# Performance work log

Measured on AMD Instinct MI355X. Metric: run time of the kernel, lower is better.

Reference implementation:

```python
import jax, jax.numpy as jnp
import numpy as np

NUM_HEADS = 16
NEG_INF = -1e18


def setup_inputs() -> dict:
    key = jax.random.key(0)
    ks = jax.random.split(key, 9)
    T, B, D = 2048, 2, 1024
    s = 1.0 / np.sqrt(D)
    return {
        "query": jax.random.normal(ks[0], (T, B, D), jnp.float32),
        "q_w": jax.random.normal(ks[1], (D, D), jnp.float32) * s,
        "q_b": jax.random.normal(ks[2], (D,), jnp.float32) * 0.02,
        "k_w": jax.random.normal(ks[3], (D, D), jnp.float32) * s,
        "k_b": jax.random.normal(ks[4], (D,), jnp.float32) * 0.02,
        "v_w": jax.random.normal(ks[5], (D, D), jnp.float32) * s,
        "v_b": jax.random.normal(ks[6], (D,), jnp.float32) * 0.02,
        "out_w": jax.random.normal(ks[7], (D, D), jnp.float32) * s,
        "out_b": jax.random.normal(ks[8], (D,), jnp.float32) * 0.02,
    }


def reference(query, q_w, q_b, k_w, k_b, v_w, v_b, out_w, out_b):
    # query: [T, B, D] (Time x Batch x Channel). Self-attention, causal mask,
    # dropout=0, need_weights=True.
    T, B, D = query.shape
    H = NUM_HEADS
    hd = D // H
    scaling = 1.0 / jnp.sqrt(jnp.asarray(hd, query.dtype))

    q = (query @ q_w.T + q_b) * scaling
    k = query @ k_w.T + k_b
    v = query @ v_w.T + v_b

    def split_heads(x):  # [T, B, D] -> [B, H, T, hd]
        return x.reshape(T, B, H, hd).transpose(1, 2, 0, 3)

    qh, kh, vh = split_heads(q), split_heads(k), split_heads(v)

    # scores: [B, H, T, T]
    scores = jnp.einsum("bhtd,bhsd->bhts", qh, kh)
    causal = jnp.triu(jnp.full((T, T), NEG_INF, dtype=scores.dtype), k=1)
    scores = scores + causal

    probs = jax.nn.softmax(scores, axis=-1)
    attn = jnp.einsum("bhts,bhsd->bhtd", probs, vh)  # [B, H, T, hd]
    attn = attn.transpose(2, 0, 1, 3).reshape(T, B, D)
    out = attn @ out_w.T + out_b

    # averaged attention weights over heads: [B, T, T]
    avg_weights = probs.sum(axis=1) / H
    return out, avg_weights
```

## Files before the change

### kernel.cpp

```cpp
#include <hip/hip_runtime.h>
#include <hip/hip_bf16.h>
#include <stdint.h>

typedef __hip_bfloat16 bf16;
using short8 = __attribute__((ext_vector_type(8))) short;
using f32x4  = __attribute__((ext_vector_type(4))) float;

#define TDIM 2048
#define BDIM 2
#define DDIM 1024
#define HNUM 16
#define HD   64
#define MDIM 4096
#define M0   16.0f

__device__ __forceinline__ f32x4 mfma16(short8 a, short8 b, f32x4 c) {
  return __builtin_amdgcn_mfma_f32_16x16x32_bf16(a, b, c, 0, 0, 0);
}

union S8 { short8 v; bf16 h[8]; };

__device__ __forceinline__ void gload16(const bf16* g, bf16* l) {
  __builtin_amdgcn_global_load_lds(
      (const __attribute__((address_space(1))) unsigned int*)g,
      (__attribute__((address_space(3))) unsigned int*)l, 16, 0, 0);
}

__global__ __launch_bounds__(256) void cast_all_kernel(
    const float* __restrict__ q, const float* __restrict__ wq,
    const float* __restrict__ wk, const float* __restrict__ wv,
    const float* __restrict__ wo, bf16* __restrict__ dst) {
  int t4 = blockIdx.x * blockDim.x + threadIdx.x;
  int idx = t4 * 4;
  const float* s;
  if (idx < 4194304)      s = q  + idx;
  else if (idx < 5242880) s = wq + (idx - 4194304);
  else if (idx < 6291456) s = wk + (idx - 5242880);
  else if (idx < 7340032) s = wv + (idx - 6291456);
  else                    s = wo + (idx - 7340032);
  float4 v = *(const float4*)s;
  union { ushort4 u; bf16 b[4]; } pk;
  pk.b[0] = __float2bfloat16(v.x);
  pk.b[1] = __float2bfloat16(v.y);
  pk.b[2] = __float2bfloat16(v.z);
  pk.b[3] = __float2bfloat16(v.w);
  *(ushort4*)(dst + idx) = pk.u;
}

__global__ __launch_bounds__(256) void qkv_kernel(
    const bf16* __restrict__ X, const bf16* __restrict__ Wq,
    const bf16* __restrict__ Wk, const bf16* __restrict__ Wv,
    const float* __restrict__ qb, const float* __restrict__ kb,
    const float* __restrict__ vb, bf16* __restrict__ Qo,
    bf16* __restrict__ Ko, bf16* __restrict__ Vto) {
  __shared__ bf16 Xs[128][64];
  __shared__ bf16 Qs[64][64];
  __shared__ bf16 Ks[64][64];
  __shared__ bf16 Vs[64][64];
  const int tid = threadIdx.x, lane = tid & 63, wave = tid >> 6;
  const int m0 = blockIdx.y * 128, n0 = blockIdx.x * 64;
  const int wm = (wave >> 1) * 64, wn = (wave & 1) * 32;
  const int fr = lane & 15, quad = lane >> 4, q8 = quad * 8;
  const int lr = lane >> 3, lc = (lane & 7) * 8;
  f32x4 aq[4][2] = {}, ak[4][2] = {}, av[2][4] = {};
  for (int k0 = 0; k0 < DDIM; k0 += 64) {
    if (k0) __syncthreads();
#pragma unroll
    for (int p = 0; p < 10; p++) {
      int pid = wave * 10 + p;
      const bf16* g;
      bf16* l;
      if (pid < 16) {
        g = X + (size_t)(m0 + pid * 8 + lr) * DDIM + k0 + lc;
        l = &Xs[pid * 8][0];
      } else if (pid < 24) {
        int r = (pid - 16) * 8;
        g = Wq + (size_t)(n0 + r + lr) * DDIM + k0 + lc;
        l = &Qs[r][0];
      } else if (pid < 32) {
        int r = (pid - 24) * 8;
        g = Wk + (size_t)(n0 + r + lr) * DDIM + k0 + lc;
        l = &Ks[r][0];
      } else {
        int r = (pid - 32) * 8;
        g = Wv + (size_t)(n0 + r + lr) * DDIM + k0 + lc;
        l = &Vs[r][0];
      }
      gload16(g, l);
    }
    __syncthreads();
#pragma unroll
    for (int kk = 0; kk < 2; kk++) {
      const int ko = kk * 32 + q8;
      short8 xf[4], qf[2], kf[2], vf[2];
#pragma unroll
      for (int i = 0; i < 4; i++)
        xf[i] = *(const short8*)&Xs[wm + i * 16 + fr][ko];
#pragma unroll
      for (int j = 0; j < 2; j++) {
        qf[j] = *(const short8*)&Qs[wn + j * 16 + fr][ko];
        kf[j] = *(const short8*)&Ks[wn + j * 16 + fr][ko];
        vf[j] = *(const short8*)&Vs[wn + j * 16 + fr][ko];
      }
#pragma unroll
      for (int i = 0; i < 4; i++)
#pragma unroll
        for (int j = 0; j < 2; j++) {
          aq[i][j] = mfma16(xf[i], qf[j], aq[i][j]);
          ak[i][j] = mfma16(xf[i], kf[j], ak[i][j]);
          av[j][i] = mfma16(vf[j], xf[i], av[j][i]);
        }
    }
  }
#pragma unroll
  for (int i = 0; i < 4; i++)
#pragma unroll
    for (int j = 0; j < 2; j++)
#pragma unroll
      for (int r = 0; r < 4; r++) {
        {
          int gm = m0 + wm + i * 16 + quad * 4 + r;
          int gn = n0 + wn + j * 16 + fr;
          int t = gm >> 1, bb = gm & 1, h = gn >> 6, e = gn & 63;
          size_t o = ((size_t)(bb * HNUM + h) * TDIM + t) * HD + e;
          Qo[o] = __float2bfloat16((aq[i][j][r] + qb[gn]) * 0.125f);
          Ko[o] = __float2bfloat16(ak[i][j][r] + kb[gn]);
        }
        {
          int gf = n0 + wn + j * 16 + quad * 4 + r;
          int gt = m0 + wm + i * 16 + fr;
          int t = gt >> 1, bb = gt & 1, h = gf >> 6, e = gf & 63;
          Vto[((size_t)(bb * HNUM + h) * HD + e) * TDIM + t] =
              __float2bfloat16(av[j][i][r] + vb[gf]);
        }
      }
}

__global__ __launch_bounds__(256) void gemm_out_kernel(
    const bf16* __restrict__ P0, const bf16* __restrict__ P1,
    const bf16* __restrict__ Bw, const float* __restrict__ l0buf,
    const float* __restrict__ l1buf, const float* __restrict__ bias,
    float* __restrict__ of32) {
  __shared__ bf16 As[64][40];
  __shared__ bf16 Bs[64][40];
  __shared__ float sInv[64][16];
  const int tid  = threadIdx.x;
  const int lane = tid & 63, wave = tid >> 6;
  const int m0 = blockIdx.y * 64, n0 = blockIdx.x * 64;
  const int wm = (wave >> 1) * 32, wn = (wave & 1) * 32;
  const int fr = lane & 15, quad = lane >> 4, q8 = quad * 8;
  const int ldr = tid >> 2, ldc = (tid & 3) * 8;
#pragma unroll
  for (int e = 0; e < 4; e++) {
    int idx = tid * 4 + e;
    int row = idx >> 4, h = idx & 15;
    int gm = m0 + row, t = gm >> 1, bb = gm & 1;
    size_t li = (size_t)(bb * HNUM + h) * TDIM + t;
    sInv[row][h] = 1.0f / (l0buf[li] + l1buf[li]);
  }
  __syncthreads();
  f32x4 acc[2][2] = {};
  const size_t arow = (size_t)(m0 + ldr) * DDIM + ldc;
  const bf16* bptr = Bw + (size_t)(n0 + ldr) * DDIM + ldc;
  for (int k0 = 0; k0 < DDIM; k0 += 32) {
    S8 a0, a1, apk;
    a0.v = *(const short8*)&P0[arow + k0];
    a1.v = *(const short8*)&P1[arow + k0];
    uint4 bvv = *(const uint4*)(bptr + k0);
    float inv = sInv[ldr][k0 >> 6];
#pragma unroll
    for (int k = 0; k < 8; k++)
      apk.h[k] = __float2bfloat16(
          (__bfloat162float(a0.h[k]) + __bfloat162float(a1.h[k])) * inv);
    __syncthreads();
    *(short8*)&As[ldr][ldc] = apk.v;
    *(uint4*)&Bs[ldr][ldc] = bvv;
    __syncthreads();
    short8 af[2], bfr[2];
    af[0]  = *(const short8*)&As[wm + fr][q8];
    af[1]  = *(const short8*)&As[wm + 16 + fr][q8];
    bfr[0] = *(const short8*)&Bs[wn + fr][q8];
    bfr[1] = *(const short8*)&Bs[wn + 16 + fr][q8];
    acc[0][0] = mfma16(af[0], bfr[0], acc[0][0]);
    acc[0][1] = mfma16(af[0], bfr[1], acc[0][1]);
    acc[1][0] = mfma16(af[1], bfr[0], acc[1][0]);
    acc[1][1] = mfma16(af[1], bfr[1], acc[1][1]);
  }
#pragma unroll
  for (int mt = 0; mt < 2; mt++)
#pragma unroll
    for (int nt = 0; nt < 2; nt++)
#pragma unroll
      for (int i = 0; i < 4; i++) {
        int gm = m0 + wm + mt * 16 + quad * 4 + i;
        int gn = n0 + wn + nt * 16 + fr;
        of32[(size_t)gm * DDIM + gn] = acc[mt][nt][i] + bias[gn];
      }
}

__global__ __launch_bounds__(256) void attn_split_kernel(
    const bf16* __restrict__ Q, const bf16* __restrict__ K,
    const bf16* __restrict__ Vt, bf16* __restrict__ P0o,
    bf16* __restrict__ P1o, float* __restrict__ l0buf,
    float* __restrict__ l1buf) {
  __shared__ bf16 Ks[2][64][40];
  __shared__ bf16 Vs[2][64][40];
  __shared__ bf16 pt[4][16][72];
  const int tid = threadIdx.x, lane = tid & 63, wave = tid >> 6;
  const int bid = blockIdx.x;
  const int part = bid & 1, bh = (bid >> 1) & 31, t64 = 31 - (bid >> 6);
  const int b = bh >> 4, h = bh & 15;
  const int t0 = t64 * 64 + wave * 16;
  const int fr = lane & 15, quad = lane >> 4, q8 = quad * 8;
  const bf16* Qp = Q + ((size_t)bh * TDIM + t0) * HD;
  const bf16* Kp = K + (size_t)bh * TDIM * HD;
  const bf16* Vp = Vt + (size_t)bh * HD * TDIM;
  short8 aq0 = *(const short8*)&Qp[fr * HD + q8];
  short8 aq1 = *(const short8*)&Qp[fr * HD + 32 + q8];
  const int Cb = t64 + 1, C0 = Cb >> 1;
  const int clo = part ? C0 : 0, chi = part ? Cb : C0;
  const int sr0 = tid >> 3, scc = (tid & 7) * 8, sr1 = sr0 + 32;
  const int ssub = scc >> 5, scol = scc & 31;
  f32x4 oacc[4] = {};
  float lsum[4] = {0.f, 0.f, 0.f, 0.f};
  uint4 kv0, kv1, vv0, vv1;
  auto ldglob = [&](int c) {
    int s0 = c * 64;
    kv0 = *(const uint4*)&Kp[(size_t)(s0 + sr0) * HD + scc];
    kv1 = *(const uint4*)&Kp[(size_t)(s0 + sr1) * HD + scc];
    vv0 = *(const uint4*)&Vp[(size_t)sr0 * TDIM + s0 + scc];
    vv1 = *(const uint4*)&Vp[(size_t)sr1 * TDIM + s0 + scc];
  };
  if (clo < chi) ldglob(clo);
  for (int c = clo; c < chi; c++) {
    __syncthreads();
    *(uint4*)&Ks[ssub][sr0][scol] = kv0;
    *(uint4*)&Ks[ssub][sr1][scol] = kv1;
    *(uint4*)&Vs[ssub][sr0][scol] = vv0;
    *(uint4*)&Vs[ssub][sr1][scol] = vv1;
    __syncthreads();
    if (c + 1 < chi) ldglob(c + 1);
    const int s0 = c * 64;
    f32x4 sc[4] = {};
#pragma unroll
    for (int j = 0; j < 4; j++) {
      short8 b0 = *(const short8*)&Ks[0][j * 16 + fr][q8];
      short8 b1 = *(const short8*)&Ks[1][j * 16 + fr][q8];
      sc[j] = mfma16(aq0, b0, sc[j]);
      sc[j] = mfma16(aq1, b1, sc[j]);
    }
#pragma unroll
    for (int j = 0; j < 4; j++) {
      int s_col = s0 + j * 16 + fr;
#pragma unroll
      for (int i = 0; i < 4; i++) {
        float p = 0.f;
        if (s_col <= t0 + quad * 4 + i) {
          p = __expf(sc[j][i] - M0);
          lsum[i] += p;
        }
        pt[wave][quad * 4 + i][j * 16 + fr] = __float2bfloat16(p);
      }
    }
    short8 ap0 = *(const short8*)&pt[wave][fr][q8];
    short8 ap1 = *(const short8*)&pt[wave][fr][32 + q8];
#pragma unroll
    for (int nt = 0; nt < 4; nt++) {
      short8 v0 = *(const short8*)&Vs[0][nt * 16 + fr][q8];
      short8 v1 = *(const short8*)&Vs[1][nt * 16 + fr][q8];
      oacc[nt] = mfma16(ap0, v0, oacc[nt]);
      oacc[nt] = mfma16(ap1, v1, oacc[nt]);
    }
  }
  float lr[4];
#pragma unroll
  for (int i = 0; i < 4; i++) {
    float l = lsum[i];
#pragma unroll
    for (int off = 1; off < 16; off <<= 1) l += __shfl_xor(l, off, 16);
    lr[i] = l;
  }
  bf16*  Op = part ? P1o : P0o;
  float* lb = part ? l1buf : l0buf;
#pragma unroll
  for (int nt = 0; nt < 4; nt++)
#pragma unroll
    for (int i = 0; i < 4; i++) {
      int t_row = t0 + quad * 4 + i;
      int col = h * HD + nt * 16 + fr;
      Op[((size_t)t_row * BDIM + b) * DDIM + col] = __float2bfloat16(oacc[nt][i]);
    }
  if (fr == 0) {
    float4 v = make_float4(lr[0], lr[1], lr[2], lr[3]);
    *(float4*)&lb[(size_t)bh * TDIM + t0 + quad * 4] = v;
  }
}

__global__ __launch_bounds__(256) void avg_kernel(
    const bf16* __restrict__ Q, const bf16* __restrict__ K,
    const float* __restrict__ l0buf, const float* __restrict__ l1buf,
    float* __restrict__ avgw) {
  const int tid = threadIdx.x;
  int r = blockIdx.x;
  const int b = (r >= 2048) ? 1 : 0;
  r &= 2047;
  float* avp = avgw + (size_t)b * TDIM * TDIM;
  if (r >= 1056) {
    int r2 = r - 1056;
    int ti = 0;
    while (ti < 31 && (ti + 1) * (62 - ti) <= r2) ti++;
    int si = (2 * ti + 2) + (r2 - ti * (63 - ti));
    int t0b = ti * 64, s0 = si * 32;
#pragma unroll
    for (int k = 0; k < 2; k++) {
      int off = (tid * 2 + k) * 4;
      *(float4*)&avp[(size_t)(t0b + (off >> 5)) * TDIM + s0 + (off & 31)] =
          make_float4(0.f, 0.f, 0.f, 0.f);
    }
    return;
  }
  int ti = 0;
  while ((ti + 1) * (ti + 2) <= r) ti++;
  const int si = r - ti * (ti + 1);
  const int t0b = ti * 64, s0 = si * 32;

  __shared__ bf16 Qs[2][64][40];
  __shared__ bf16 Ks2[2][32][40];
  __shared__ float sinvl[HNUM][64];
#pragma unroll
  for (int k = 0; k < 4; k++) {
    int idx = tid + k * 256;
    size_t li = (size_t)(b * HNUM + (idx >> 6)) * TDIM + t0b + (idx & 63);
    sinvl[idx >> 6][idx & 63] = 1.0f / (l0buf[li] + l1buf[li]);
  }
  const int lane = tid & 63, wave = tid >> 6;
  const int fr = lane & 15, quad = lane >> 4, q8 = quad * 8;
  const int twr = wave * 16;
  const int qr0 = tid >> 3, qcc = (tid & 7) * 8, qr1 = qr0 + 32;
  const int qsub = qcc >> 5, qcol = qcc & 31;
  const bf16* Qb = Q + (size_t)b * HNUM * TDIM * HD;
  const bf16* Kb = K + (size_t)b * HNUM * TDIM * HD;
  uint4 qv0, qv1, kv1;
  auto ldh = [&](int hh) {
    const bf16* Qh = Qb + (size_t)hh * TDIM * HD;
    const bf16* Kh = Kb + (size_t)hh * TDIM * HD;
    qv0 = *(const uint4*)&Qh[(size_t)(t0b + qr0) * HD + qcc];
    qv1 = *(const uint4*)&Qh[(size_t)(t0b + qr1) * HD + qcc];
    kv1 = *(const uint4*)&Kh[(size_t)(s0 + (qr0 & 31)) * HD + qcc];
  };
  ldh(0);
  f32x4 facc[2] = {};
  for (int hh = 0; hh < HNUM; hh++) {
    __syncthreads();
    *(uint4*)&Qs[qsub][qr0][qcol] = qv0;
    *(uint4*)&Qs[qsub][qr1][qcol] = qv1;
    if (qr0 < 32) *(uint4*)&Ks2[qsub][qr0][qcol] = kv1;
    else          *(uint4*)&Ks2[qsub][qr0 - 32][qcol] = kv1;
    __syncthreads();
    if (hh + 1 < HNUM) ldh(hh + 1);
    short8 a0 = *(const short8*)&Qs[0][twr + fr][q8];
    short8 a1 = *(const short8*)&Qs[1][twr + fr][q8];
#pragma unroll
    for (int nt = 0; nt < 2; nt++) {
      short8 b0 = *(const short8*)&Ks2[0][nt * 16 + fr][q8];
      short8 b1 = *(const short8*)&Ks2[1][nt * 16 + fr][q8];
      f32x4 sc = {};
      sc = mfma16(a0, b0, sc);
      sc = mfma16(a1, b1, sc);
#pragma unroll
      for (int i = 0; i < 4; i++) {
        int tr = twr + quad * 4 + i;
        if (s0 + nt * 16 + fr <= t0b + tr)
          facc[nt][i] += __expf(sc[i] - M0) * sinvl[hh][tr];
      }
    }
  }
#pragma unroll
  for (int nt = 0; nt < 2; nt++)
#pragma unroll
    for (int i = 0; i < 4; i++)
      avp[(size_t)(t0b + twr + quad * 4 + i) * TDIM + s0 + nt * 16 + fr] =
          facc[nt][i] * 0.0625f;
}

extern "C" void kernel_launch(void* const* d_in, const int* in_sizes, int n_in,
                              void* d_out, int out_size, void* d_ws, size_t ws_size,
                              hipStream_t stream) {
  const float* q   = (const float*)d_in[0];
  const float* q_w = (const float*)d_in[1];
  const float* q_b = (const float*)d_in[2];
  const float* k_w = (const float*)d_in[3];
  const float* k_b = (const float*)d_in[4];
  const float* v_w = (const float*)d_in[5];
  const float* v_b = (const float*)d_in[6];
  const float* o_w = (const float*)d_in[7];
  const float* o_b = (const float*)d_in[8];
  float* out = (float*)d_out;
  float* avg = out + (size_t)MDIM * DDIM;

  bf16* ws  = (bf16*)d_ws;
  bf16* Xbf = ws;
  bf16* Wq  = ws + 4194304;
  bf16* Wk  = ws + 5242880;
  bf16* Wv  = ws + 6291456;
  bf16* Wo  = ws + 7340032;
  bf16* Qw  = ws + 8388608;
  bf16* Kw  = ws + 12582912;
  bf16* Vt  = ws + 16777216;
  bf16* P1  = ws + 20971520;
  bf16* P0  = ws;
  float* l0 = (float*)(ws + 4194304);
  float* l1 = (float*)(ws + 4325376);

  cast_all_kernel<<<8192, 256, 0, stream>>>(q, q_w, k_w, v_w, o_w, Xbf);
  qkv_kernel<<<dim3(16, 32), 256, 0, stream>>>(Xbf, Wq, Wk, Wv, q_b, k_b, v_b,
                                               Qw, Kw, Vt);
  attn_split_kernel<<<2048, 256, 0, stream>>>(Qw, Kw, Vt, P0, P1, l0, l1);
  avg_kernel<<<4096, 256, 0, stream>>>(Qw, Kw, l0, l1, avg);
  gemm_out_kernel<<<dim3(16, 64), 256, 0, stream>>>(P0, P1, Wo, l0, l1, o_b, out);
}
```

Baseline: 265.4 us.

## Enlarge attention query tile, transpose score MFMA, and rework QKV tiling

```diff
diff --git a/kernel.cpp b/kernel.cpp
--- a/kernel.cpp
+++ b/kernel.cpp
@@ -19,12 +19,7 @@
 }
 
 union S8 { short8 v; bf16 h[8]; };
-
-__device__ __forceinline__ void gload16(const bf16* g, bf16* l) {
-  __builtin_amdgcn_global_load_lds(
-      (const __attribute__((address_space(1))) unsigned int*)g,
-      (__attribute__((address_space(3))) unsigned int*)l, 16, 0, 0);
-}
+union P4 { uint2 u; bf16 h[4]; };
 
 __global__ __launch_bounds__(256) void cast_all_kernel(
     const float* __restrict__ q, const float* __restrict__ wq,
@@ -53,85 +48,77 @@
     const float* __restrict__ qb, const float* __restrict__ kb,
     const float* __restrict__ vb, bf16* __restrict__ Qo,
     bf16* __restrict__ Ko, bf16* __restrict__ Vto) {
-  __shared__ bf16 Xs[128][64];
-  __shared__ bf16 Qs[64][64];
-  __shared__ bf16 Ks[64][64];
-  __shared__ bf16 Vs[64][64];
-  const int tid = threadIdx.x, lane = tid & 63, wave = tid >> 6;
-  const int m0 = blockIdx.y * 128, n0 = blockIdx.x * 64;
-  const int wm = (wave >> 1) * 64, wn = (wave & 1) * 32;
+  __shared__ __align__(16) bf16 Xs[64][72];
+  __shared__ __align__(16) bf16 Qs[64][72];
+  __shared__ __align__(16) bf16 Ks[64][72];
+  __shared__ __align__(16) bf16 Vs[64][72];
+  const int tid  = threadIdx.x;
+  const int lane = tid & 63, wave = tid >> 6;
+  const int m0 = blockIdx.y * 64, n0 = blockIdx.x * 64;
+  const int wm = (wave >> 1) * 32, wn = (wave & 1) * 32;
   const int fr = lane & 15, quad = lane >> 4, q8 = quad * 8;
-  const int lr = lane >> 3, lc = (lane & 7) * 8;
-  f32x4 aq[4][2] = {}, ak[4][2] = {}, av[2][4] = {};
+  const int r = tid >> 3, cc = (tid & 7) * 8;
+  f32x4 aq[2][2] = {}, ak[2][2] = {}, av[2][2] = {};
+  const bf16* xp0 = X  + (size_t)(m0 + r) * DDIM + cc;
+  const bf16* xp1 = xp0 + 32 * DDIM;
+  const bf16* qp0 = Wq + (size_t)(n0 + r) * DDIM + cc;
+  const bf16* qp1 = qp0 + 32 * DDIM;
+  const bf16* kp0 = Wk + (size_t)(n0 + r) * DDIM + cc;
+  const bf16* kp1 = kp0 + 32 * DDIM;
+  const bf16* vp0 = Wv + (size_t)(n0 + r) * DDIM + cc;
+  const bf16* vp1 = vp0 + 32 * DDIM;
   for (int k0 = 0; k0 < DDIM; k0 += 64) {
-    if (k0) __syncthreads();
-#pragma unroll
-    for (int p = 0; p < 10; p++) {
-      int pid = wave * 10 + p;
-      const bf16* g;
-      bf16* l;
-      if (pid < 16) {
-        g = X + (size_t)(m0 + pid * 8 + lr) * DDIM + k0 + lc;
-        l = &Xs[pid * 8][0];
-      } else if (pid < 24) {
-        int r = (pid - 16) * 8;
-        g = Wq + (size_t)(n0 + r + lr) * DDIM + k0 + lc;
-        l = &Qs[r][0];
-      } else if (pid < 32) {
-        int r = (pid - 24) * 8;
-        g = Wk + (size_t)(n0 + r + lr) * DDIM + k0 + lc;
-        l = &Ks[r][0];
-      } else {
-        int r = (pid - 32) * 8;
-        g = Wv + (size_t)(n0 + r + lr) * DDIM + k0 + lc;
-        l = &Vs[r][0];
-      }
-      gload16(g, l);
-    }
+    uint4 xv0 = *(const uint4*)(xp0 + k0), xv1 = *(const uint4*)(xp1 + k0);
+    uint4 qv0 = *(const uint4*)(qp0 + k0), qv1 = *(const uint4*)(qp1 + k0);
+    uint4 kv0 = *(const uint4*)(kp0 + k0), kv1 = *(const uint4*)(kp1 + k0);
+    uint4 vv0 = *(const uint4*)(vp0 + k0), vv1 = *(const uint4*)(vp1 + k0);
+    __syncthreads();
+    *(uint4*)&Xs[r][cc] = xv0; *(uint4*)&Xs[r + 32][cc] = xv1;
+    *(uint4*)&Qs[r][cc] = qv0; *(uint4*)&Qs[r + 32][cc] = qv1;
+    *(uint4*)&Ks[r][cc] = kv0; *(uint4*)&Ks[r + 32][cc] = kv1;
+    *(uint4*)&Vs[r][cc] = vv0; *(uint4*)&Vs[r + 32][cc] = vv1;
     __syncthreads();
 #pragma unroll
     for (int kk = 0; kk < 2; kk++) {
       const int ko = kk * 32 + q8;
-      short8 xf[4], qf[2], kf[2], vf[2];
-#pragma unroll
-      for (int i = 0; i < 4; i++)
-        xf[i] = *(const short8*)&Xs[wm + i * 16 + fr][ko];
+      short8 xf[2], qf[2], kf[2], vf[2];
 #pragma unroll
       for (int j = 0; j < 2; j++) {
+        xf[j] = *(const short8*)&Xs[wm + j * 16 + fr][ko];
         qf[j] = *(const short8*)&Qs[wn + j * 16 + fr][ko];
         kf[j] = *(const short8*)&Ks[wn + j * 16 + fr][ko];
         vf[j] = *(const short8*)&Vs[wn + j * 16 + fr][ko];
       }
 #pragma unroll
-      for (int i = 0; i < 4; i++)
+      for (int i = 0; i < 2; i++)
 #pragma unroll
         for (int j = 0; j < 2; j++) {
           aq[i][j] = mfma16(xf[i], qf[j], aq[i][j]);
           ak[i][j] = mfma16(xf[i], kf[j], ak[i][j]);
-          av[j][i] = mfma16(vf[j], xf[i], av[j][i]);
+          av[i][j] = mfma16(vf[i], xf[j], av[i][j]);
         }
     }
   }
 #pragma unroll
-  for (int i = 0; i < 4; i++)
-#pragma unroll
-    for (int j = 0; j < 2; j++)
-#pragma unroll
-      for (int r = 0; r < 4; r++) {
+  for (int mt = 0; mt < 2; mt++)
+#pragma unroll
+    for (int nt = 0; nt < 2; nt++)
+#pragma unroll
+      for (int i = 0; i < 4; i++) {
         {
-          int gm = m0 + wm + i * 16 + quad * 4 + r;
-          int gn = n0 + wn + j * 16 + fr;
+          int gm = m0 + wm + mt * 16 + quad * 4 + i;
+          int gn = n0 + wn + nt * 16 + fr;
           int t = gm >> 1, bb = gm & 1, h = gn >> 6, e = gn & 63;
           size_t o = ((size_t)(bb * HNUM + h) * TDIM + t) * HD + e;
-          Qo[o] = __float2bfloat16((aq[i][j][r] + qb[gn]) * 0.125f);
-          Ko[o] = __float2bfloat16(ak[i][j][r] + kb[gn]);
+          Qo[o] = __float2bfloat16((aq[mt][nt][i] + qb[gn]) * 0.125f);
+          Ko[o] = __float2bfloat16(ak[mt][nt][i] + kb[gn]);
         }
         {
-          int gf = n0 + wn + j * 16 + quad * 4 + r;
-          int gt = m0 + wm + i * 16 + fr;
+          int gf = n0 + wn + mt * 16 + quad * 4 + i;
+          int gt = m0 + wm + nt * 16 + fr;
           int t = gt >> 1, bb = gt & 1, h = gf >> 6, e = gf & 63;
           Vto[((size_t)(bb * HNUM + h) * HD + e) * TDIM + t] =
-              __float2bfloat16(av[j][i][r] + vb[gf]);
+              __float2bfloat16(av[mt][nt][i] + vb[gf]);
         }
       }
 }
@@ -141,8 +128,8 @@
     const bf16* __restrict__ Bw, const float* __restrict__ l0buf,
     const float* __restrict__ l1buf, const float* __restrict__ bias,
     float* __restrict__ of32) {
-  __shared__ bf16 As[64][40];
-  __shared__ bf16 Bs[64][40];
+  __shared__ __align__(16) bf16 As[64][40];
+  __shared__ __align__(16) bf16 Bs[64][40];
   __shared__ float sInv[64][16];
   const int tid  = threadIdx.x;
   const int lane = tid & 63, wave = tid >> 6;
@@ -203,26 +190,29 @@
     const bf16* __restrict__ Vt, bf16* __restrict__ P0o,
     bf16* __restrict__ P1o, float* __restrict__ l0buf,
     float* __restrict__ l1buf) {
-  __shared__ bf16 Ks[2][64][40];
-  __shared__ bf16 Vs[2][64][40];
-  __shared__ bf16 pt[4][16][72];
+  __shared__ __align__(16) bf16 Ks[2][64][40];
+  __shared__ __align__(16) bf16 Vs[2][64][40];
+  __shared__ __align__(16) bf16 pt[4][32][72];
   const int tid = threadIdx.x, lane = tid & 63, wave = tid >> 6;
   const int bid = blockIdx.x;
-  const int part = bid & 1, bh = (bid >> 1) & 31, t64 = 31 - (bid >> 6);
+  const int part = bid & 1, bh = (bid >> 1) & 31, t128 = 15 - (bid >> 6);
   const int b = bh >> 4, h = bh & 15;
-  const int t0 = t64 * 64 + wave * 16;
+  const int t0 = t128 * 128 + wave * 32;
   const int fr = lane & 15, quad = lane >> 4, q8 = quad * 8;
   const bf16* Qp = Q + ((size_t)bh * TDIM + t0) * HD;
   const bf16* Kp = K + (size_t)bh * TDIM * HD;
   const bf16* Vp = Vt + (size_t)bh * HD * TDIM;
-  short8 aq0 = *(const short8*)&Qp[fr * HD + q8];
-  short8 aq1 = *(const short8*)&Qp[fr * HD + 32 + q8];
-  const int Cb = t64 + 1, C0 = Cb >> 1;
+  short8 aq[2][2];
+  aq[0][0] = *(const short8*)&Qp[fr * HD + q8];
+  aq[0][1] = *(const short8*)&Qp[fr * HD + 32 + q8];
+  aq[1][0] = *(const short8*)&Qp[(16 + fr) * HD + q8];
+  aq[1][1] = *(const short8*)&Qp[(16 + fr) * HD + 32 + q8];
+  const int Cb = 2 * t128 + 2, C0 = t128 + 1;
   const int clo = part ? C0 : 0, chi = part ? Cb : C0;
   const int sr0 = tid >> 3, scc = (tid & 7) * 8, sr1 = sr0 + 32;
   const int ssub = scc >> 5, scol = scc & 31;
-  f32x4 oacc[4] = {};
-  float lsum[4] = {0.f, 0.f, 0.f, 0.f};
+  f32x4 oacc[2][4] = {};
+  float lsum[2] = {0.f, 0.f};
   uint4 kv0, kv1, vv0, vv1;
   auto ldglob = [&](int c) {
     int s0 = c * 64;
@@ -231,7 +221,7 @@
     vv0 = *(const uint4*)&Vp[(size_t)sr0 * TDIM + s0 + scc];
     vv1 = *(const uint4*)&Vp[(size_t)sr1 * TDIM + s0 + scc];
   };
-  if (clo < chi) ldglob(clo);
+  ldglob(clo);
   for (int c = clo; c < chi; c++) {
     __syncthreads();
     *(uint4*)&Ks[ssub][sr0][scol] = kv0;
@@ -241,58 +231,71 @@
     __syncthreads();
     if (c + 1 < chi) ldglob(c + 1);
     const int s0 = c * 64;
-    f32x4 sc[4] = {};
+    f32x4 scT[2][4] = {};
 #pragma unroll
     for (int j = 0; j < 4; j++) {
-      short8 b0 = *(const short8*)&Ks[0][j * 16 + fr][q8];
-      short8 b1 = *(const short8*)&Ks[1][j * 16 + fr][q8];
-      sc[j] = mfma16(aq0, b0, sc[j]);
-      sc[j] = mfma16(aq1, b1, sc[j]);
-    }
-#pragma unroll
-    for (int j = 0; j < 4; j++) {
-      int s_col = s0 + j * 16 + fr;
-#pragma unroll
-      for (int i = 0; i < 4; i++) {
-        float p = 0.f;
-        if (s_col <= t0 + quad * 4 + i) {
-          p = __expf(sc[j][i] - M0);
-          lsum[i] += p;
+      short8 k0f = *(const short8*)&Ks[0][j * 16 + fr][q8];
+      short8 k1f = *(const short8*)&Ks[1][j * 16 + fr][q8];
+      scT[0][j] = mfma16(k0f, aq[0][0], scT[0][j]);
+      scT[0][j] = mfma16(k1f, aq[0][1], scT[0][j]);
+      scT[1][j] = mfma16(k0f, aq[1][0], scT[1][j]);
+      scT[1][j] = mfma16(k1f, aq[1][1], scT[1][j]);
+    }
+#pragma unroll
+    for (int g = 0; g < 2; g++) {
+      const int t_row = t0 + g * 16 + fr;
+#pragma unroll
+      for (int j = 0; j < 4; j++) {
+        const int s_base = s0 + j * 16 + quad * 4;
+        P4 pk;
+#pragma unroll
+        for (int i = 0; i < 4; i++) {
+          float p = 0.f;
+          if (s_base + i <= t_row) {
+            p = __expf(scT[g][j][i] - M0);
+            lsum[g] += p;
+          }
+          pk.h[i] = __float2bfloat16(p);
         }
-        pt[wave][quad * 4 + i][j * 16 + fr] = __float2bfloat16(p);
-      }
-    }
-    short8 ap0 = *(const short8*)&pt[wave][fr][q8];
-    short8 ap1 = *(const short8*)&pt[wave][fr][32 + q8];
-#pragma unroll
-    for (int nt = 0; nt < 4; nt++) {
-      short8 v0 = *(const short8*)&Vs[0][nt * 16 + fr][q8];
-      short8 v1 = *(const short8*)&Vs[1][nt * 16 + fr][q8];
-      oacc[nt] = mfma16(ap0, v0, oacc[nt]);
-      oacc[nt] = mfma16(ap1, v1, oacc[nt]);
-    }
-  }
-  float lr[4];
-#pragma unroll
-  for (int i = 0; i < 4; i++) {
-    float l = lsum[i];
-#pragma unroll
-    for (int off = 1; off < 16; off <<= 1) l += __shfl_xor(l, off, 16);
-    lr[i] = l;
+        *(uint2*)&pt[wave][g * 16 + fr][j * 16 + quad * 4] = pk.u;
+      }
+    }
+#pragma unroll
+    for (int c2 = 0; c2 < 2; c2++) {
+      short8 ap0 = *(const short8*)&pt[wave][fr][c2 * 32 + q8];
+      short8 ap1 = *(const short8*)&pt[wave][16 + fr][c2 * 32 + q8];
+#pragma unroll
+      for (int nt = 0; nt < 4; nt++) {
+        short8 vf = *(const short8*)&Vs[c2][nt * 16 + fr][q8];
+        oacc[0][nt] = mfma16(ap0, vf, oacc[0][nt]);
+        oacc[1][nt] = mfma16(ap1, vf, oacc[1][nt]);
+      }
+    }
+  }
+  float lr[2];
+#pragma unroll
+  for (int g = 0; g < 2; g++) {
+    float l = lsum[g];
+    l += __shfl_xor(l, 16);
+    l += __shfl_xor(l, 32);
+    lr[g] = l;
   }
   bf16*  Op = part ? P1o : P0o;
   float* lb = part ? l1buf : l0buf;
 #pragma unroll
-  for (int nt = 0; nt < 4; nt++)
-#pragma unroll
-    for (int i = 0; i < 4; i++) {
-      int t_row = t0 + quad * 4 + i;
-      int col = h * HD + nt * 16 + fr;
-      Op[((size_t)t_row * BDIM + b) * DDIM + col] = __float2bfloat16(oacc[nt][i]);
-    }
-  if (fr == 0) {
-    float4 v = make_float4(lr[0], lr[1], lr[2], lr[3]);
-    *(float4*)&lb[(size_t)bh * TDIM + t0 + quad * 4] = v;
+  for (int g = 0; g < 2; g++)
+#pragma unroll
+    for (int nt = 0; nt < 4; nt++)
+#pragma unroll
+      for (int i = 0; i < 4; i++) {
+        int t_row = t0 + g * 16 + quad * 4 + i;
+        int col = h * HD + nt * 16 + fr;
+        Op[((size_t)t_row * BDIM + b) * DDIM + col] =
+            __float2bfloat16(oacc[g][nt][i]);
+      }
+  if (quad == 0) {
+    lb[(size_t)bh * TDIM + t0 + fr]      = lr[0];
+    lb[(size_t)bh * TDIM + t0 + 16 + fr] = lr[1];
   }
 }
 
@@ -324,8 +327,8 @@
   const int si = r - ti * (ti + 1);
   const int t0b = ti * 64, s0 = si * 32;
 
-  __shared__ bf16 Qs[2][64][40];
-  __shared__ bf16 Ks2[2][32][40];
+  __shared__ __align__(16) bf16 Qs[2][64][40];
+  __shared__ __align__(16) bf16 Ks2[2][32][40];
   __shared__ float sinvl[HNUM][64];
 #pragma unroll
   for (int k = 0; k < 4; k++) {
@@ -413,9 +416,9 @@
   float* l1 = (float*)(ws + 4325376);
 
   cast_all_kernel<<<8192, 256, 0, stream>>>(q, q_w, k_w, v_w, o_w, Xbf);
-  qkv_kernel<<<dim3(16, 32), 256, 0, stream>>>(Xbf, Wq, Wk, Wv, q_b, k_b, v_b,
+  qkv_kernel<<<dim3(16, 64), 256, 0, stream>>>(Xbf, Wq, Wk, Wv, q_b, k_b, v_b,
                                                Qw, Kw, Vt);
-  attn_split_kernel<<<2048, 256, 0, stream>>>(Qw, Kw, Vt, P0, P1, l0, l1);
+  attn_split_kernel<<<1024, 256, 0, stream>>>(Qw, Kw, Vt, P0, P1, l0, l1);
   avg_kernel<<<4096, 256, 0, stream>>>(Qw, Kw, l0, l1, avg);
   gemm_out_kernel<<<dim3(16, 64), 256, 0, stream>>>(P0, P1, Wo, l0, l1, o_b, out);
 }
```

Result: faster. 255.8 us (-3.6%).
